# Kernel tuning notes

Hardware: AMD Instinct MI355X
Metric: run time of the kernel (lower is better)

The kernel has to match this reference:

```python
import jax, jax.numpy as jnp
import numpy as np

DIM = 768
HEADS = 12
HIDDEN = 3072  # dim * mlp_ratio
EPS = 1e-5


def layernorm(x, g, b):
    mu = jnp.mean(x, axis=-1, keepdims=True)
    var = jnp.var(x, axis=-1, keepdims=True)
    return (x - mu) * jax.lax.rsqrt(var + EPS) * g + b


def setup_inputs() -> dict:
    key = jax.random.key(0)
    ks = jax.random.split(key, 10)
    s = 0.02
    return {
        "x": jax.random.normal(ks[0], (4, 1024, DIM), jnp.float32),
        "attention_mask": jax.random.randint(ks[1], (4, 1024), 0, 2, jnp.int32),
        "ln1_g": jnp.ones((DIM,), jnp.float32),
        "ln1_b": jnp.zeros((DIM,), jnp.float32),
        "ln2_g": jnp.ones((DIM,), jnp.float32),
        "ln2_b": jnp.zeros((DIM,), jnp.float32),
        "w_qkv": jax.random.normal(ks[2], (DIM, 3 * DIM), jnp.float32) * s,
        "b_qkv": jnp.zeros((3 * DIM,), jnp.float32),
        "w_proj": jax.random.normal(ks[3], (DIM, DIM), jnp.float32) * s,
        "b_proj": jnp.zeros((DIM,), jnp.float32),
        "w_fc1": jax.random.normal(ks[4], (DIM, HIDDEN), jnp.float32) * s,
        "b_fc1": jnp.zeros((HIDDEN,), jnp.float32),
        "w_fc2": jax.random.normal(ks[5], (HIDDEN, DIM), jnp.float32) * s,
        "b_fc2": jnp.zeros((DIM,), jnp.float32),
    }


def reference(x, attention_mask, ln1_g, ln1_b, ln2_g, ln2_b,
              w_qkv, b_qkv, w_proj, b_proj, w_fc1, b_fc1, w_fc2, b_fc2):
    B, N, C = x.shape
    hd = C // HEADS
    scale = hd ** -0.5

    # --- attention branch ---
    h = layernorm(x, ln1_g, ln1_b)
    qkv = (h @ w_qkv + b_qkv).reshape(B, N, 3, HEADS, hd)
    q, k, v = qkv[:, :, 0], qkv[:, :, 1], qkv[:, :, 2]  # [B,N,H,hd]
    attn = jnp.einsum('bnhd,bmhd->bhnm', q, k) * scale
    mask_bias = jnp.where(attention_mask == 0, -10000.0, 0.0)[:, None, None, :]
    attn = jax.nn.softmax(attn + mask_bias, axis=-1)
    o = jnp.einsum('bhnm,bmhd->bnhd', attn, v).reshape(B, N, C)
    x = x + (o @ w_proj + b_proj)

    # --- MLP branch ---
    h = layernorm(x, ln2_g, ln2_b)
    h = jax.nn.gelu(h @ w_fc1 + b_fc1, approximate=False)
    x = x + (h @ w_fc2 + b_fc2)
    return x
```

## Files before the change

### kernel.cpp

```cpp
#include <hip/hip_runtime.h>

#define DIM 768
#define NTOK 4096
#define HID 3072

typedef __attribute__((ext_vector_type(8))) short bf16x8;
typedef __attribute__((ext_vector_type(4))) float f32x4;

__device__ inline unsigned short f2bf(float f){
  unsigned u = __float_as_uint(f);
  u += 0x7fff + ((u >> 16) & 1);
  return (unsigned short)(u >> 16);
}
__device__ inline unsigned cvt_pk_bf16(float a, float b){
  unsigned r;
  asm("v_cvt_pk_bf16_f32 %0, %1, %2" : "=v"(r) : "v"(a), "v"(b));
  return r;
}
__device__ inline void gload_lds16(const void* g, void* l){
  __builtin_amdgcn_global_load_lds(
      (const __attribute__((address_space(1))) unsigned int*)g,
      (__attribute__((address_space(3))) unsigned int*)l, 16, 0, 0);
}
template<int N> __device__ inline void wait_vmcnt(){
  if constexpr (N == 0) asm volatile("s_waitcnt vmcnt(0)" ::: "memory");
  else if constexpr (N == 4) asm volatile("s_waitcnt vmcnt(4)" ::: "memory");
  else if constexpr (N == 8) asm volatile("s_waitcnt vmcnt(8)" ::: "memory");
  else static_assert(N == 0, "unsupported vmcnt");
}
__device__ inline int swz_read(int row, int hi){
  return (row * 64 + hi * 16) ^ ((row & 7) << 4);
}

__global__ __launch_bounds__(256) void ln_kernel(const float* __restrict__ x,
    const float* __restrict__ g, const float* __restrict__ b,
    unsigned short* __restrict__ out)
{
  int row = blockIdx.x * 4 + (threadIdx.x >> 6);
  int lane = threadIdx.x & 63;
  const float* xr = x + (size_t)row * DIM;
  float4 v[3];
  float s = 0.f, s2 = 0.f;
#pragma unroll
  for (int j = 0; j < 3; ++j){
    v[j] = *(const float4*)(xr + j * 256 + lane * 4);
    s  += v[j].x + v[j].y + v[j].z + v[j].w;
    s2 += v[j].x*v[j].x + v[j].y*v[j].y + v[j].z*v[j].z + v[j].w*v[j].w;
  }
#pragma unroll
  for (int m = 1; m < 64; m <<= 1){ s += __shfl_xor(s, m, 64); s2 += __shfl_xor(s2, m, 64); }
  float mu  = s * (1.f / 768.f);
  float var = s2 * (1.f / 768.f) - mu * mu;
  float inv = rsqrtf(var + 1e-5f);
#pragma unroll
  for (int j = 0; j < 3; ++j){
    int c0 = j * 256 + lane * 4;
    float vv[4] = { v[j].x, v[j].y, v[j].z, v[j].w };
    ushort4 o4;
    o4.x = f2bf((vv[0] - mu) * inv * g[c0 + 0] + b[c0 + 0]);
    o4.y = f2bf((vv[1] - mu) * inv * g[c0 + 1] + b[c0 + 1]);
    o4.z = f2bf((vv[2] - mu) * inv * g[c0 + 2] + b[c0 + 2]);
    o4.w = f2bf((vv[3] - mu) * inv * g[c0 + 3] + b[c0 + 3]);
    *(ushort4*)(out + (size_t)row * DIM + c0) = o4;
  }
}

__global__ __launch_bounds__(256) void transpose4_kernel(
    const float* __restrict__ w_qkv, const float* __restrict__ w_proj,
    const float* __restrict__ w_fc1, const float* __restrict__ w_fc2,
    unsigned short* __restrict__ tq, unsigned short* __restrict__ tp,
    unsigned short* __restrict__ t1, unsigned short* __restrict__ t2)
{
  __shared__ __align__(16) unsigned short tile[32][33];
  int id = blockIdx.x;
  const float* W; unsigned short* Wt; int K, N, tx_n;
  if (id < 1728)      { W = w_qkv;  Wt = tq; K = 768;  N = 2304; tx_n = 72; }
  else if (id < 2304) { W = w_proj; Wt = tp; K = 768;  N = 768;  tx_n = 24; id -= 1728; }
  else if (id < 4608) { W = w_fc1;  Wt = t1; K = 768;  N = 3072; tx_n = 96; id -= 2304; }
  else                { W = w_fc2;  Wt = t2; K = 3072; N = 768;  tx_n = 24; id -= 4608; }
  int n0 = (id % tx_n) * 32, k0 = (id / tx_n) * 32;
  int tx = threadIdx.x & 31, ty = threadIdx.x >> 5;
#pragma unroll
  for (int i = 0; i < 32; i += 8)
    tile[ty + i][tx] = f2bf(W[(size_t)(k0 + ty + i) * N + n0 + tx]);
  __syncthreads();
#pragma unroll
  for (int i = 0; i < 32; i += 8)
    Wt[(size_t)(n0 + ty + i) * K + k0 + tx] = tile[tx][ty + i];
}

__global__ __launch_bounds__(256) void pack_mask_kernel(const int* __restrict__ am,
    unsigned long long* __restrict__ pm)
{
  int lane = threadIdx.x & 63, w = threadIdx.x >> 6, b = blockIdx.x;
  for (int k = w; k < 16; k += 4){
    unsigned long long m = __ballot(am[b * 1024 + k * 64 + lane] != 0);
    if (lane == 0) pm[b * 16 + k] = m;
  }
}

template<int EPI, typename OutT>
__global__ __launch_bounds__(256) void gemm_kernel(
    const unsigned short* __restrict__ A,
    const unsigned short* __restrict__ Bt,
    const float* __restrict__ bias,
    OutT* __restrict__ C,
    unsigned short* __restrict__ q_out,
    unsigned short* __restrict__ k_out,
    unsigned short* __restrict__ v_out,
    int M, int N, int K)
{
  constexpr int BM = 128, BN = 128, BK = 32, WM = 64, WN = 64, DEPTH = 3;
  constexpr int MI = WM / 16, NI = WN / 16;
  constexpr int SMEM_B = DEPTH * (BM + BN) * BK * 2;
  __shared__ __align__(16) char smem[SMEM_B];
  auto As = (unsigned short(*)[BM * BK])smem;
  auto Bs = (unsigned short(*)[BN * BK])(smem + DEPTH * BM * BK * 2);
  const int t = threadIdx.x, lane = t & 63, wid = t >> 6;
  const int lo = lane & 15, hi = lane >> 4;
  const int wr = wid >> 1, wc = wid & 1;

  const int gx = gridDim.x;
  const int nwg = gx * gridDim.y;
  const int lin = blockIdx.y * gx + blockIdx.x;
  const int swz = (lin & 7) * (nwg >> 3) + (lin >> 3);
  const int bm = (swz / gx) * BM, bn = (swz % gx) * BN;

  const unsigned short *a0, *a1, *b0, *b1;
  {
    int rp = t >> 2, r = rp ^ ((rp >> 2) & 1), q = (t & 3) ^ (r & 3);
    a0 = A  + (size_t)(bm + r) * K + q * 8;
    b0 = Bt + (size_t)(bn + r) * K + q * 8;
    int c = 256 + t;
    rp = c >> 2; r = rp ^ ((rp >> 2) & 1); q = (c & 3) ^ (r & 3);
    a1 = A  + (size_t)(bm + r) * K + q * 8;
    b1 = Bt + (size_t)(bn + r) * K + q * 8;
  }
  int ofsA[MI], ofsB[NI];
#pragma unroll
  for (int i = 0; i < MI; ++i) ofsA[i] = swz_read(wr * WM + i * 16 + lo, hi);
#pragma unroll
  for (int j = 0; j < NI; ++j) ofsB[j] = swz_read(wc * WN + j * 16 + lo, hi);

  f32x4 acc[MI][NI];
#pragma unroll
  for (int i = 0; i < MI; ++i)
#pragma unroll
    for (int j = 0; j < NI; ++j) acc[i][j] = (f32x4){0.f, 0.f, 0.f, 0.f};

  const int NIT = K / BK;
  auto stagefull = [&](int buf) __attribute__((always_inline)) {
    gload_lds16(a0, &As[buf][t * 8]);
    gload_lds16(a1, &As[buf][(256 + t) * 8]);
    gload_lds16(b0, &Bs[buf][t * 8]);
    gload_lds16(b1, &Bs[buf][(256 + t) * 8]);
    a0 += BK; a1 += BK; b0 += BK; b1 += BK;
  };
  auto kbody = [&](int it, int RB, int WB) __attribute__((always_inline)) {
    if (it < NIT - 1) wait_vmcnt<4>(); else wait_vmcnt<0>();
    __builtin_amdgcn_sched_barrier(0);
    __builtin_amdgcn_s_barrier();
    __builtin_amdgcn_sched_barrier(0);
    if (it + 2 < NIT) stagefull(WB);
    const char* as = (const char*)As[RB];
    const char* bs = (const char*)Bs[RB];
    bf16x8 af[MI], bfr[NI];
#pragma unroll
    for (int i = 0; i < MI; ++i) af[i]  = *(const bf16x8*)(as + ofsA[i]);
#pragma unroll
    for (int j = 0; j < NI; ++j) bfr[j] = *(const bf16x8*)(bs + ofsB[j]);
#pragma unroll
    for (int i = 0; i < MI; ++i)
#pragma unroll
      for (int j = 0; j < NI; ++j)
        acc[i][j] = __builtin_amdgcn_mfma_f32_16x16x32_bf16(af[i], bfr[j], acc[i][j], 0, 0, 0);
  };

  stagefull(0);
  stagefull(1);
  for (int it = 0; it < NIT; it += 3){
    kbody(it,     0, 2);
    kbody(it + 1, 1, 0);
    kbody(it + 2, 2, 1);
  }

  __syncthreads();

  if constexpr (EPI == 0 || EPI == 1){
    constexpr int LDE = BN + 8;
    unsigned short* ET = (unsigned short*)smem;
#pragma unroll
    for (int i = 0; i < MI; ++i)
#pragma unroll
      for (int j = 0; j < NI; ++j){
        float bcol = bias[bn + wc * WN + j * 16 + lo];
#pragma unroll
        for (int r = 0; r < 4; ++r){
          float v = acc[i][j][r] + bcol;
          if constexpr (EPI == 1) v = 0.5f * v * (1.f + erff(v * 0.70710678118f));
          ET[(wr * WM + i * 16 + hi * 4 + r) * LDE + wc * WN + j * 16 + lo] = f2bf(v);
        }
      }
    __syncthreads();
#pragma unroll
    for (int p = 0; p < BM / 16; ++p){
      int row = p * 16 + (t >> 4), chunk = t & 15;
      *(bf16x8*)&((unsigned short*)C)[(size_t)(bm + row) * N + bn + chunk * 8] =
          *(const bf16x8*)&ET[row * LDE + chunk * 8];
    }
  } else {
    constexpr int LDE = BN + 8;
    unsigned short* ET = (unsigned short*)smem;
    const int part = bn / 768;
    const int cloc = bn % 768;
#pragma unroll
    for (int i = 0; i < MI; ++i)
#pragma unroll
      for (int j = 0; j < NI; ++j){
        int col_l = wc * WN + j * 16 + lo;
        float bcol = bias[bn + col_l];
#pragma unroll
        for (int r = 0; r < 4; ++r){
          int row_l = wr * WM + i * 16 + hi * 4 + r;
          unsigned short us = f2bf(acc[i][j][r] + bcol);
          if (part < 2) ET[row_l * LDE + col_l] = us;
          else          ET[col_l * LDE + row_l] = us;
        }
      }
    __syncthreads();
    const int bb = bm >> 10, n0b = bm & 1023;
    if (part < 2){
      unsigned short* dst0 = (part == 0) ? q_out : k_out;
#pragma unroll
      for (int p = 0; p < 8; ++p){
        int row = p * 16 + (t >> 4), chunk = t & 15;
        int hh = cloc / 64 + (chunk >> 3), d0 = (chunk & 7) * 8;
        unsigned short* dst = dst0 + ((size_t)(bb * 12 + hh)) * 65536 + (n0b + row) * 64 + d0;
        *(bf16x8*)dst = *(const bf16x8*)&ET[row * LDE + chunk * 8];
      }
    } else {
#pragma unroll
      for (int p = 0; p < 8; ++p){
        int colg = p * 16 + (t >> 4), chunk = t & 15;
        int hh = cloc / 64 + (colg >> 6), d = colg & 63;
        unsigned short* dst = v_out + ((size_t)(bb * 12 + hh)) * 65536 + (size_t)d * 1024 + n0b + chunk * 8;
        *(bf16x8*)dst = *(const bf16x8*)&ET[colg * LDE + chunk * 8];
      }
    }
  }
}

__global__ __launch_bounds__(512) void gemm_ks_kernel(
    const unsigned short* __restrict__ A,
    const unsigned short* __restrict__ Bt,
    const float* __restrict__ bias,
    const float* __restrict__ resid,
    float* __restrict__ C,
    int M, int N, int K)
{
  constexpr int BM = 128, BN = 96, BK = 64, DEPTH = 3;
  constexpr int MI = 4, NI = 3;
  constexpr int ACH = BM * BK / 8;
  constexpr int BCH = BN * BK / 8;
  constexpr int NC = 4;
  constexpr int TILE_A = BM * BK * 2, TILE_B = BN * BK * 2;
  constexpr int LDE = BN + 4;
  constexpr int SMEM_B = (DEPTH * (TILE_A + TILE_B) > BM * LDE * 4)
                       ?  DEPTH * (TILE_A + TILE_B) : BM * LDE * 4;
  __shared__ __align__(16) char smem[SMEM_B];
  auto As = (unsigned short(*)[BM * BK])smem;
  auto Bs = (unsigned short(*)[BN * BK])(smem + DEPTH * TILE_A);
  const int t = threadIdx.x, lane = t & 63, wid = t >> 6;
  const int lo = lane & 15, hi = lane >> 4;
  const int ks = wid & 1, wc = (wid >> 1) & 1, wr = wid >> 2;

  const int gx = gridDim.x;
  const int nwg = gx * gridDim.y;
  const int lin = blockIdx.y * gx + blockIdx.x;
  const int swz = (lin & 7) * (nwg >> 3) + (lin >> 3);
  const int bm = (swz / gx) * BM, bn = (swz % gx) * BN;

  auto stage = [&](int buf, int k0){
#pragma unroll
    for (int u = 0; u < NC; ++u){
      int c = u * 512 + t;
      if (c < ACH){
        int r = c >> 3, q = (c & 7) ^ (r & 7);
        gload_lds16(A + (size_t)(bm + r) * K + k0 + q * 8, &As[buf][c * 8]);
      } else {
        int c2 = c - ACH;
        if (c2 >= BCH) c2 -= BCH;
        int r = c2 >> 3, q = (c2 & 7) ^ (r & 7);
        gload_lds16(Bt + (size_t)(bn + r) * K + k0 + q * 8, &Bs[buf][c2 * 8]);
      }
    }
  };
  auto rd = [&](const char* base, int row, int q)->bf16x8 {
    return *(const bf16x8*)(base + row * 128 + ((q ^ (row & 7)) << 4));
  };

  f32x4 acc[MI][NI];
#pragma unroll
  for (int i = 0; i < MI; ++i)
#pragma unroll
    for (int j = 0; j < NI; ++j) acc[i][j] = (f32x4){0.f, 0.f, 0.f, 0.f};

  const int NIT = K / BK;
  stage(0, 0);
  stage(1, BK);
  const int qk = ks * 4 + hi;
  for (int it = 0; it < NIT; ++it){
    if (it < NIT - 1) wait_vmcnt<NC>();
    else wait_vmcnt<0>();
    __builtin_amdgcn_sched_barrier(0);
    __builtin_amdgcn_s_barrier();
    __builtin_amdgcn_sched_barrier(0);
    if (it + 2 < NIT) stage((it + 2) % DEPTH, (it + 2) * BK);
    const char* as = (const char*)As[it % DEPTH];
    const char* bs = (const char*)Bs[it % DEPTH];
    bf16x8 af[MI], bfr[NI];
#pragma unroll
    for (int i = 0; i < MI; ++i)  af[i]  = rd(as, wr * 64 + i * 16 + lo, qk);
#pragma unroll
    for (int j = 0; j < NI; ++j) bfr[j] = rd(bs, wc * 48 + j * 16 + lo, qk);
#pragma unroll
    for (int i = 0; i < MI; ++i)
#pragma unroll
      for (int j = 0; j < NI; ++j)
        acc[i][j] = __builtin_amdgcn_mfma_f32_16x16x32_bf16(af[i], bfr[j], acc[i][j], 0, 0, 0);
  }

  __syncthreads();
  float* ET = (float*)smem;
  if (ks == 1){
#pragma unroll
    for (int i = 0; i < MI; ++i)
#pragma unroll
      for (int j = 0; j < NI; ++j)
#pragma unroll
        for (int r = 0; r < 4; ++r)
          ET[(wr * 64 + i * 16 + hi * 4 + r) * LDE + wc * 48 + j * 16 + lo] = acc[i][j][r];
  }
  __syncthreads();
  if (ks == 0){
#pragma unroll
    for (int i = 0; i < MI; ++i)
#pragma unroll
      for (int j = 0; j < NI; ++j){
        int col_l = wc * 48 + j * 16 + lo;
        float bcol = bias[bn + col_l];
#pragma unroll
        for (int r = 0; r < 4; ++r){
          int idx = (wr * 64 + i * 16 + hi * 4 + r) * LDE + col_l;
          ET[idx] = ET[idx] + acc[i][j][r] + bcol;
        }
      }
  }
  __syncthreads();
  {
    int row = t >> 2, q = t & 3;
    const float* rrow = resid + (size_t)(bm + row) * N + bn;
    float* crow = C + (size_t)(bm + row) * N + bn;
#pragma unroll
    for (int k = 0; k < 6; ++k){
      int c4 = (q + k * 4) * 4;
      float4 v = *(const float4*)&ET[row * LDE + c4];
      float4 rs = *(const float4*)&rrow[c4];
      v.x += rs.x; v.y += rs.y; v.z += rs.z; v.w += rs.w;
      *(float4*)&crow[c4] = v;
    }
  }
}

__global__ __launch_bounds__(256) void attn_kernel(
    const unsigned short* __restrict__ Qs,
    const unsigned short* __restrict__ Ks,
    const unsigned short* __restrict__ Vts,
    const unsigned long long* __restrict__ pm,
    unsigned short* __restrict__ o)
{
  constexpr int LD = 72;
  __shared__ __align__(16) unsigned short Kl[2][64 * LD];
  __shared__ __align__(16) unsigned short Vt[2][64 * LD];
  __shared__ __align__(16) unsigned short Pl[4][16 * LD];
  const int qb = blockIdx.x, h = blockIdx.y, b = blockIdx.z;
  const int t = threadIdx.x, wid = t >> 6, lane = t & 63;
  const int lo = lane & 15, hi = lane >> 4;
  const size_t bh = (size_t)b * 12 + h;

  const unsigned short* Qg = Qs + (bh * 1024 + qb * 64 + wid * 16 + lo) * 64;
  bf16x8 qf0 = *(const bf16x8*)(Qg + hi * 8);
  bf16x8 qf1 = *(const bf16x8*)(Qg + 32 + hi * 8);

  f32x4 oacc[4];
#pragma unroll
  for (int dj = 0; dj < 4; ++dj) oacc[dj] = (f32x4){0.f, 0.f, 0.f, 0.f};
  float l_part = 0.f;

  const int srow = t >> 2, scol = (t & 3) * 16;
  const int sdst = srow * LD + scol;
  const unsigned short* kg = Ks  + bh * 65536 + srow * 64 + scol;
  const unsigned short* vg = Vts + bh * 65536 + srow * 1024 + scol;
  unsigned short* pw = &Pl[wid][0];

  bf16x8 kn0 = *(const bf16x8*)(kg);
  bf16x8 kn1 = *(const bf16x8*)(kg + 8);
  bf16x8 vn0 = *(const bf16x8*)(vg);
  bf16x8 vn1 = *(const bf16x8*)(vg + 8);
  *(bf16x8*)&Kl[0][sdst]     = kn0;
  *(bf16x8*)&Kl[0][sdst + 8] = kn1;
  *(bf16x8*)&Vt[0][sdst]     = vn0;
  *(bf16x8*)&Vt[0][sdst + 8] = vn1;
  __syncthreads();

  for (int kt = 0; kt < 16; ++kt){
    const int cur = kt & 1;
    if (kt + 1 < 16){
      kn0 = *(const bf16x8*)(kg + (kt + 1) * 4096);
      kn1 = *(const bf16x8*)(kg + (kt + 1) * 4096 + 8);
      vn0 = *(const bf16x8*)(vg + (kt + 1) * 64);
      vn1 = *(const bf16x8*)(vg + (kt + 1) * 64 + 8);
    }

    f32x4 s[4];
#pragma unroll
    for (int nj = 0; nj < 4; ++nj) s[nj] = (f32x4){0.f, 0.f, 0.f, 0.f};
#pragma unroll
    for (int kk = 0; kk < 2; ++kk){
      bf16x8 q = kk ? qf1 : qf0;
#pragma unroll
      for (int nj = 0; nj < 4; ++nj){
        bf16x8 kf = *(const bf16x8*)&Kl[cur][(nj * 16 + lo) * LD + kk * 32 + hi * 8];
        s[nj] = __builtin_amdgcn_mfma_f32_16x16x32_bf16(kf, q, s[nj], 0, 0, 0);
      }
    }

    unsigned long long w = pm[b * 16 + kt] >> (hi * 4);
#pragma unroll
    for (int nj = 0; nj < 4; ++nj){
      float p[4];
#pragma unroll
      for (int r = 0; r < 4; ++r){
        float e = __expf(fmaf(s[nj][r], 0.125f, -16.0f));
        e = ((unsigned)(w >> (nj * 16 + r)) & 1u) ? e : 0.0f;
        l_part += e;
        p[r] = e;
      }
      unsigned w0 = cvt_pk_bf16(p[0], p[1]);
      unsigned w1 = cvt_pk_bf16(p[2], p[3]);
      *(uint2*)&pw[lo * LD + nj * 16 + hi * 4] = make_uint2(w0, w1);
    }
    asm volatile("" ::: "memory");
    bf16x8 pf0 = *(const bf16x8*)&pw[lo * LD + hi * 8];
    bf16x8 pf1 = *(const bf16x8*)&pw[lo * LD + 32 + hi * 8];
#pragma unroll
    for (int kk = 0; kk < 2; ++kk){
      bf16x8 pf = kk ? pf1 : pf0;
#pragma unroll
      for (int dj = 0; dj < 4; ++dj){
        bf16x8 vf = *(const bf16x8*)&Vt[cur][(dj * 16 + lo) * LD + kk * 32 + hi * 8];
        oacc[dj] = __builtin_amdgcn_mfma_f32_16x16x32_bf16(vf, pf, oacc[dj], 0, 0, 0);
      }
    }

    if (kt + 1 < 16){
      *(bf16x8*)&Kl[cur ^ 1][sdst]     = kn0;
      *(bf16x8*)&Kl[cur ^ 1][sdst + 8] = kn1;
      *(bf16x8*)&Vt[cur ^ 1][sdst]     = vn0;
      *(bf16x8*)&Vt[cur ^ 1][sdst + 8] = vn1;
    }
    __syncthreads();
  }

  float l = l_part;
  l += __shfl_xor(l, 16, 64);
  l += __shfl_xor(l, 32, 64);
  float inv = 1.0f / l;
  size_t orow = (size_t)b * 1024 + qb * 64 + wid * 16 + lo;
#pragma unroll
  for (int dj = 0; dj < 4; ++dj){
    unsigned w0 = (unsigned)f2bf(oacc[dj][0] * inv) | ((unsigned)f2bf(oacc[dj][1] * inv) << 16);
    unsigned w1 = (unsigned)f2bf(oacc[dj][2] * inv) | ((unsigned)f2bf(oacc[dj][3] * inv) << 16);
    *(uint2*)&o[orow * DIM + h * 64 + dj * 16 + hi * 4] = make_uint2(w0, w1);
  }
}

extern "C" void kernel_launch(void* const* d_in, const int* in_sizes, int n_in,
                              void* d_out, int out_size, void* d_ws, size_t ws_size,
                              hipStream_t stream)
{
  const float* x      = (const float*)d_in[0];
  const int*   amask  = (const int*)  d_in[1];
  const float* ln1_g  = (const float*)d_in[2];
  const float* ln1_b  = (const float*)d_in[3];
  const float* ln2_g  = (const float*)d_in[4];
  const float* ln2_b  = (const float*)d_in[5];
  const float* w_qkv  = (const float*)d_in[6];
  const float* b_qkv  = (const float*)d_in[7];
  const float* w_proj = (const float*)d_in[8];
  const float* b_proj = (const float*)d_in[9];
  const float* w_fc1  = (const float*)d_in[10];
  const float* b_fc1  = (const float*)d_in[11];
  const float* w_fc2  = (const float*)d_in[12];
  const float* b_fc2  = (const float*)d_in[13];
  float* outp = (float*)d_out;

  char* w = (char*)d_ws;
  auto alloc = [&](size_t bytes){ char* p = w; w += (bytes + 255) & ~(size_t)255; return p; };

  char* p0 = alloc((size_t)4 * 6291456);
  unsigned short* Qs   = (unsigned short*)p0;
  unsigned short* Ks   = (unsigned short*)(p0 + 6291456);
  unsigned short* Vts  = (unsigned short*)(p0 + 2 * 6291456);
  unsigned short* o_bf = (unsigned short*)(p0 + 3 * 6291456);
  unsigned short* a1   = (unsigned short*)p0;
  unsigned short* h_bf = (unsigned short*)alloc((size_t)NTOK * DIM * 2);
  unsigned short* h2   = h_bf;
  float*          x1   = (float*)alloc((size_t)NTOK * DIM * 4);
  unsigned short* wqkvT = (unsigned short*)alloc((size_t)3 * DIM * DIM * 2);
  unsigned short* wprojT= (unsigned short*)alloc((size_t)DIM * DIM * 2);
  unsigned short* wfc1T = (unsigned short*)alloc((size_t)HID * DIM * 2);
  unsigned short* wfc2T = (unsigned short*)alloc((size_t)DIM * HID * 2);
  unsigned long long* pmask = (unsigned long long*)alloc(4 * 16 * 8);

  transpose4_kernel<<<6912, 256, 0, stream>>>(w_qkv, w_proj, w_fc1, w_fc2,
                                              wqkvT, wprojT, wfc1T, wfc2T);
  pack_mask_kernel<<<4, 256, 0, stream>>>(amask, pmask);

  ln_kernel<<<NTOK / 4, 256, 0, stream>>>(x, ln1_g, ln1_b, h_bf);
  gemm_kernel<3, unsigned short><<<dim3(2304 / 128, NTOK / 128), 256, 0, stream>>>(
      h_bf, wqkvT, b_qkv, (unsigned short*)nullptr, Qs, Ks, Vts, NTOK, 2304, DIM);
  attn_kernel<<<dim3(16, 12, 4), 256, 0, stream>>>(Qs, Ks, Vts, pmask, o_bf);
  gemm_ks_kernel<<<dim3(8, NTOK / 128), 512, 0, stream>>>(
      o_bf, wprojT, b_proj, x, x1, NTOK, DIM, DIM);
  ln_kernel<<<NTOK / 4, 256, 0, stream>>>(x1, ln2_g, ln2_b, h2);
  gemm_kernel<1, unsigned short><<<dim3(HID / 128, NTOK / 128), 256, 0, stream>>>(
      h2, wfc1T, b_fc1, a1, nullptr, nullptr, nullptr, NTOK, HID, DIM);
  gemm_ks_kernel<<<dim3(8, NTOK / 128), 512, 0, stream>>>(
      a1, wfc2T, b_fc2, x1, outp, NTOK, DIM, HID);
}
```

Baseline: 160.8 us.

## Use 128x96 tiles for QKV GEMM and split-K kernel for FC1 GELU

The QKV GEMM moves from 128x128 to 128x96 tiles, giving 24x32=768 workgroups instead of 576. Its B-tile staging and its Q/K/V scatter epilogue are reworked to fit the narrower tile. FC1 now runs through the 512-thread split-K gemm_ks kernel with a new bf16 GELU epilogue, also on 128x96 tiles (1024 workgroups). The aim is better CU occupancy and wave balance on the 256-CU part. The cost is uneven per-thread B loads in the QKV kernel, a 12-of-16 active-lane store pattern, and split-K reduction overhead on FC1.

Result: slower. 171.1 us (+6.4%).

```diff
diff --git a/kernel.cpp b/kernel.cpp
--- a/kernel.cpp
+++ b/kernel.cpp
@@ -99,19 +99,17 @@
   }
 }
 
-template<int EPI, typename OutT>
-__global__ __launch_bounds__(256) void gemm_kernel(
+__global__ __launch_bounds__(256) void gemm_qkv_kernel(
     const unsigned short* __restrict__ A,
     const unsigned short* __restrict__ Bt,
     const float* __restrict__ bias,
-    OutT* __restrict__ C,
     unsigned short* __restrict__ q_out,
     unsigned short* __restrict__ k_out,
     unsigned short* __restrict__ v_out,
     int M, int N, int K)
 {
-  constexpr int BM = 128, BN = 128, BK = 32, WM = 64, WN = 64, DEPTH = 3;
-  constexpr int MI = WM / 16, NI = WN / 16;
+  constexpr int BM = 128, BN = 96, BK = 32, DEPTH = 3;
+  constexpr int MI = 4, NI = 3;
   constexpr int SMEM_B = DEPTH * (BM + BN) * BK * 2;
   __shared__ __align__(16) char smem[SMEM_B];
   auto As = (unsigned short(*)[BM * BK])smem;
@@ -126,21 +124,26 @@
   const int swz = (lin & 7) * (nwg >> 3) + (lin >> 3);
   const int bm = (swz / gx) * BM, bn = (swz % gx) * BN;
 
-  const unsigned short *a0, *a1, *b0, *b1;
+  const unsigned short *p0, *p1, *p2, *p3;
+  int d3;
   {
-    int rp = t >> 2, r = rp ^ ((rp >> 2) & 1), q = (t & 3) ^ (r & 3);
-    a0 = A  + (size_t)(bm + r) * K + q * 8;
-    b0 = Bt + (size_t)(bn + r) * K + q * 8;
-    int c = 256 + t;
-    rp = c >> 2; r = rp ^ ((rp >> 2) & 1); q = (c & 3) ^ (r & 3);
-    a1 = A  + (size_t)(bm + r) * K + q * 8;
-    b1 = Bt + (size_t)(bn + r) * K + q * 8;
+    int c, rp, r, q;
+    c = t;       rp = c >> 2; r = rp ^ ((rp >> 2) & 1); q = (c & 3) ^ (r & 3);
+    p0 = A  + (size_t)(bm + r) * K + q * 8;
+    c = 256 + t; rp = c >> 2; r = rp ^ ((rp >> 2) & 1); q = (c & 3) ^ (r & 3);
+    p1 = A  + (size_t)(bm + r) * K + q * 8;
+    c = t;       rp = c >> 2; r = rp ^ ((rp >> 2) & 1); q = (c & 3) ^ (r & 3);
+    p2 = Bt + (size_t)(bn + r) * K + q * 8;
+    int c2w = (t < 128) ? 256 + t : t - 128;
+    c = c2w;     rp = c >> 2; r = rp ^ ((rp >> 2) & 1); q = (c & 3) ^ (r & 3);
+    p3 = Bt + (size_t)(bn + r) * K + q * 8;
+    d3 = c2w * 8;
   }
   int ofsA[MI], ofsB[NI];
 #pragma unroll
-  for (int i = 0; i < MI; ++i) ofsA[i] = swz_read(wr * WM + i * 16 + lo, hi);
-#pragma unroll
-  for (int j = 0; j < NI; ++j) ofsB[j] = swz_read(wc * WN + j * 16 + lo, hi);
+  for (int i = 0; i < MI; ++i) ofsA[i] = swz_read(wr * 64 + i * 16 + lo, hi);
+#pragma unroll
+  for (int j = 0; j < NI; ++j) ofsB[j] = swz_read(wc * 48 + j * 16 + lo, hi);
 
   f32x4 acc[MI][NI];
 #pragma unroll
@@ -150,11 +153,11 @@
 
   const int NIT = K / BK;
   auto stagefull = [&](int buf) __attribute__((always_inline)) {
-    gload_lds16(a0, &As[buf][t * 8]);
-    gload_lds16(a1, &As[buf][(256 + t) * 8]);
-    gload_lds16(b0, &Bs[buf][t * 8]);
-    gload_lds16(b1, &Bs[buf][(256 + t) * 8]);
-    a0 += BK; a1 += BK; b0 += BK; b1 += BK;
+    gload_lds16(p0, &As[buf][t * 8]);
+    gload_lds16(p1, &As[buf][(256 + t) * 8]);
+    gload_lds16(p2, &Bs[buf][t * 8]);
+    gload_lds16(p3, &Bs[buf][d3]);
+    p0 += BK; p1 += BK; p2 += BK; p3 += BK;
   };
   auto kbody = [&](int it, int RB, int WB) __attribute__((always_inline)) {
     if (it < NIT - 1) wait_vmcnt<4>(); else wait_vmcnt<0>();
@@ -186,76 +189,63 @@
 
   __syncthreads();
 
-  if constexpr (EPI == 0 || EPI == 1){
-    constexpr int LDE = BN + 8;
-    unsigned short* ET = (unsigned short*)smem;
+  const int part = bn / 768;
+  const int cloc = bn % 768;
+  const int bb = bm >> 10, n0b = bm & 1023;
+  unsigned short* ET = (unsigned short*)smem;
+  if (part < 2){
+    constexpr int LDE = 104;
 #pragma unroll
     for (int i = 0; i < MI; ++i)
 #pragma unroll
       for (int j = 0; j < NI; ++j){
-        float bcol = bias[bn + wc * WN + j * 16 + lo];
-#pragma unroll
-        for (int r = 0; r < 4; ++r){
-          float v = acc[i][j][r] + bcol;
-          if constexpr (EPI == 1) v = 0.5f * v * (1.f + erff(v * 0.70710678118f));
-          ET[(wr * WM + i * 16 + hi * 4 + r) * LDE + wc * WN + j * 16 + lo] = f2bf(v);
-        }
+        int col_l = wc * 48 + j * 16 + lo;
+        float bcol = bias[bn + col_l];
+#pragma unroll
+        for (int r = 0; r < 4; ++r)
+          ET[(wr * 64 + i * 16 + hi * 4 + r) * LDE + col_l] = f2bf(acc[i][j][r] + bcol);
       }
     __syncthreads();
-#pragma unroll
-    for (int p = 0; p < BM / 16; ++p){
+    unsigned short* dst0 = (part == 0) ? q_out : k_out;
+#pragma unroll
+    for (int p = 0; p < 8; ++p){
       int row = p * 16 + (t >> 4), chunk = t & 15;
-      *(bf16x8*)&((unsigned short*)C)[(size_t)(bm + row) * N + bn + chunk * 8] =
-          *(const bf16x8*)&ET[row * LDE + chunk * 8];
+      if (chunk < 12){
+        int col = cloc + chunk * 8, hh = col >> 6, d0 = col & 63;
+        *(bf16x8*)&dst0[((size_t)(bb * 12 + hh)) * 65536 + (n0b + row) * 64 + d0] =
+            *(const bf16x8*)&ET[row * LDE + chunk * 8];
+      }
     }
   } else {
-    constexpr int LDE = BN + 8;
-    unsigned short* ET = (unsigned short*)smem;
-    const int part = bn / 768;
-    const int cloc = bn % 768;
+    constexpr int LDV = 136;
 #pragma unroll
     for (int i = 0; i < MI; ++i)
 #pragma unroll
       for (int j = 0; j < NI; ++j){
-        int col_l = wc * WN + j * 16 + lo;
+        int col_l = wc * 48 + j * 16 + lo;
         float bcol = bias[bn + col_l];
 #pragma unroll
-        for (int r = 0; r < 4; ++r){
-          int row_l = wr * WM + i * 16 + hi * 4 + r;
-          unsigned short us = f2bf(acc[i][j][r] + bcol);
-          if (part < 2) ET[row_l * LDE + col_l] = us;
-          else          ET[col_l * LDE + row_l] = us;
-        }
+        for (int r = 0; r < 4; ++r)
+          ET[col_l * LDV + wr * 64 + i * 16 + hi * 4 + r] = f2bf(acc[i][j][r] + bcol);
       }
     __syncthreads();
-    const int bb = bm >> 10, n0b = bm & 1023;
-    if (part < 2){
-      unsigned short* dst0 = (part == 0) ? q_out : k_out;
-#pragma unroll
-      for (int p = 0; p < 8; ++p){
-        int row = p * 16 + (t >> 4), chunk = t & 15;
-        int hh = cloc / 64 + (chunk >> 3), d0 = (chunk & 7) * 8;
-        unsigned short* dst = dst0 + ((size_t)(bb * 12 + hh)) * 65536 + (n0b + row) * 64 + d0;
-        *(bf16x8*)dst = *(const bf16x8*)&ET[row * LDE + chunk * 8];
-      }
-    } else {
-#pragma unroll
-      for (int p = 0; p < 8; ++p){
-        int colg = p * 16 + (t >> 4), chunk = t & 15;
-        int hh = cloc / 64 + (colg >> 6), d = colg & 63;
-        unsigned short* dst = v_out + ((size_t)(bb * 12 + hh)) * 65536 + (size_t)d * 1024 + n0b + chunk * 8;
-        *(bf16x8*)dst = *(const bf16x8*)&ET[colg * LDE + chunk * 8];
-      }
-    }
-  }
-}
-
+#pragma unroll
+    for (int p = 0; p < 6; ++p){
+      int colg = p * 16 + (t >> 4), chunk = t & 15;
+      int col = cloc + colg, hh = col >> 6, d = col & 63;
+      *(bf16x8*)&v_out[((size_t)(bb * 12 + hh)) * 65536 + (size_t)d * 1024 + n0b + chunk * 8] =
+          *(const bf16x8*)&ET[colg * LDV + chunk * 8];
+    }
+  }
+}
+
+template<int EPI>
 __global__ __launch_bounds__(512) void gemm_ks_kernel(
     const unsigned short* __restrict__ A,
     const unsigned short* __restrict__ Bt,
     const float* __restrict__ bias,
     const float* __restrict__ resid,
-    float* __restrict__ C,
+    void* __restrict__ Cout,
     int M, int N, int K)
 {
   constexpr int BM = 128, BN = 96, BK = 64, DEPTH = 3;
@@ -357,10 +347,10 @@
       }
   }
   __syncthreads();
-  {
+  if constexpr (EPI == 2){
     int row = t >> 2, q = t & 3;
     const float* rrow = resid + (size_t)(bm + row) * N + bn;
-    float* crow = C + (size_t)(bm + row) * N + bn;
+    float* crow = (float*)Cout + (size_t)(bm + row) * N + bn;
 #pragma unroll
     for (int k = 0; k < 6; ++k){
       int c4 = (q + k * 4) * 4;
@@ -368,6 +358,23 @@
       float4 rs = *(const float4*)&rrow[c4];
       v.x += rs.x; v.y += rs.y; v.z += rs.z; v.w += rs.w;
       *(float4*)&crow[c4] = v;
+    }
+  } else {
+    int row = t >> 2, cq = t & 3;
+    unsigned short* crow = (unsigned short*)Cout + (size_t)(bm + row) * N + bn;
+#pragma unroll
+    for (int s = 0; s < 3; ++s){
+      int c0 = cq * 8 + s * 32;
+      unsigned w4[4];
+#pragma unroll
+      for (int e = 0; e < 4; ++e){
+        float x0 = ET[row * LDE + c0 + e * 2];
+        float x1 = ET[row * LDE + c0 + e * 2 + 1];
+        x0 = 0.5f * x0 * (1.f + erff(x0 * 0.70710678118f));
+        x1 = 0.5f * x1 * (1.f + erff(x1 * 0.70710678118f));
+        w4[e] = (unsigned)f2bf(x0) | ((unsigned)f2bf(x1) << 16);
+      }
+      *(uint4*)&crow[c0] = make_uint4(w4[0], w4[1], w4[2], w4[3]);
     }
   }
 }
@@ -528,14 +535,14 @@
   pack_mask_kernel<<<4, 256, 0, stream>>>(amask, pmask);
 
   ln_kernel<<<NTOK / 4, 256, 0, stream>>>(x, ln1_g, ln1_b, h_bf);
-  gemm_kernel<3, unsigned short><<<dim3(2304 / 128, NTOK / 128), 256, 0, stream>>>(
-      h_bf, wqkvT, b_qkv, (unsigned short*)nullptr, Qs, Ks, Vts, NTOK, 2304, DIM);
+  gemm_qkv_kernel<<<dim3(2304 / 96, NTOK / 128), 256, 0, stream>>>(
+      h_bf, wqkvT, b_qkv, Qs, Ks, Vts, NTOK, 2304, DIM);
   attn_kernel<<<dim3(16, 12, 4), 256, 0, stream>>>(Qs, Ks, Vts, pmask, o_bf);
-  gemm_ks_kernel<<<dim3(8, NTOK / 128), 512, 0, stream>>>(
+  gemm_ks_kernel<2><<<dim3(DIM / 96, NTOK / 128), 512, 0, stream>>>(
       o_bf, wprojT, b_proj, x, x1, NTOK, DIM, DIM);
   ln_kernel<<<NTOK / 4, 256, 0, stream>>>(x1, ln2_g, ln2_b, h2);
-  gemm_kernel<1, unsigned short><<<dim3(HID / 128, NTOK / 128), 256, 0, stream>>>(
-      h2, wfc1T, b_fc1, a1, nullptr, nullptr, nullptr, NTOK, HID, DIM);
-  gemm_ks_kernel<<<dim3(8, NTOK / 128), 512, 0, stream>>>(
+  gemm_ks_kernel<1><<<dim3(HID / 96, NTOK / 128), 512, 0, stream>>>(
+      h2, wfc1T, b_fc1, nullptr, a1, NTOK, HID, DIM);
+  gemm_ks_kernel<2><<<dim3(DIM / 96, NTOK / 128), 512, 0, stream>>>(
       a1, wfc2T, b_fc2, x1, outp, NTOK, DIM, HID);
 }
```
